# Kernel optimization log

Hardware: AMD Instinct MI355X
Metric: run time of the kernel (lower is better)

Reference implementation:

```python
import jax, jax.numpy as jnp
import numpy as np

DIM = 1024
NUM_HEADS = 16
HEAD_DIM = DIM // NUM_HEADS
EPS = 1e-6


def _rmsnorm(x, w):
    # x: [B,H,N,D], w: [D]
    var = jnp.mean(x * x, axis=-1, keepdims=True)
    return x * jax.lax.rsqrt(var + EPS) * w


def _rotary(x, cos, sin):
    # x: [B,H,N,D]; cos/sin: [1,1,N,D/2]; complex-pair rotation (llama style)
    x2 = x.reshape(*x.shape[:-1], HEAD_DIM // 2, 2)
    xr, xi = x2[..., 0], x2[..., 1]
    or_ = xr * cos - xi * sin
    oi_ = xr * sin + xi * cos
    return jnp.stack([or_, oi_], axis=-1).reshape(x.shape)


def setup_inputs() -> dict:
    key = jax.random.key(0)
    ks = jax.random.split(key, 6)
    B, N = 2, 2048
    x = jax.random.normal(ks[0], (B, N, DIM), dtype=jnp.float32)
    pos = jax.random.uniform(ks[1], (N, HEAD_DIM // 2), dtype=jnp.float32)  # rotary angles
    s_in = 1.0 / np.sqrt(DIM)
    qkv_w = jax.random.normal(ks[2], (3 * DIM, DIM), dtype=jnp.float32) * s_in
    q_norm_w = jnp.ones((HEAD_DIM,), dtype=jnp.float32)
    k_norm_w = jnp.ones((HEAD_DIM,), dtype=jnp.float32)
    proj_w = jax.random.normal(ks[3], (DIM, DIM), dtype=jnp.float32) * s_in
    proj_b = jnp.zeros((DIM,), dtype=jnp.float32)
    return {"x": x, "pos": pos, "qkv_w": qkv_w, "q_norm_w": q_norm_w,
            "k_norm_w": k_norm_w, "proj_w": proj_w, "proj_b": proj_b}


def reference(x, pos, qkv_w, q_norm_w, k_norm_w, proj_w, proj_b):
    B, N, C = x.shape
    H, D = NUM_HEADS, HEAD_DIM
    scale = D ** -0.5
    # QKV projection: [B,N,3C] -> [3,B,H,N,D]
    qkv = jnp.einsum('bnc,fc->bnf', x, qkv_w)
    qkv = qkv.reshape(B, N, 3, H, D).transpose(2, 0, 3, 1, 4)
    q, k, v = qkv[0], qkv[1], qkv[2]
    # QK RMSNorm over head_dim
    q = _rmsnorm(q, q_norm_w)
    k = _rmsnorm(k, k_norm_w)
    # Rotary embedding (freqs_cis = exp(i * pos))
    cos = jnp.cos(pos)[None, None, :, :]
    sin = jnp.sin(pos)[None, None, :, :]
    q = _rotary(q, cos, sin)
    k = _rotary(k, cos, sin)
    # Scaled dot-product attention (non-causal)
    scores = jnp.einsum('bhnd,bhmd->bhnm', q, k) * scale
    attn = jax.nn.softmax(scores, axis=-1)
    out = jnp.einsum('bhnm,bhmd->bhnd', attn, v)
    out = out.transpose(0, 2, 1, 3).reshape(B, N, C)
    return jnp.einsum('bnc,oc->bno', out, proj_w) + proj_b
```

## Files before the change

### kernel.cpp

```cpp
#include <hip/hip_runtime.h>
#include <hip/hip_bf16.h>

typedef unsigned short ushort_t;
using floatx4 = __attribute__((__ext_vector_type__(4))) float;
using bf16x8  = __attribute__((__ext_vector_type__(8))) __bf16;
using ushort4v = __attribute__((__ext_vector_type__(4))) ushort_t;

__device__ __forceinline__ unsigned int pkbf(float a, float b) {
  __hip_bfloat162 h = __float22bfloat162_rn(make_float2(a, b));
  unsigned int u;
  __builtin_memcpy(&u, &h, 4);
  return u;
}

__device__ __forceinline__ void gl2lds16(const ushort_t* g, ushort_t* l) {
  __builtin_amdgcn_global_load_lds(
      (const __attribute__((address_space(1))) unsigned int*)g,
      (__attribute__((address_space(3))) unsigned int*)l, 16, 0, 0);
}

__global__ void cast_all(const float* __restrict__ x, const float* __restrict__ qw,
                         const float* __restrict__ pw, ushort_t* __restrict__ ob,
                         const float* __restrict__ pos, float* __restrict__ cs) {
  const int T1 = 4096 * 1024, T2 = T1 + 3072 * 1024, T3 = T2 + 1024 * 1024;
  const int tid = blockIdx.x * blockDim.x + threadIdx.x;
  if (tid < 65536) {
    const float a = pos[tid];
    cs[2 * tid]     = __cosf(a);
    cs[2 * tid + 1] = __sinf(a);
  }
  const int i = tid * 4;
  if (i < T3) {
    const float* src = (i < T1) ? (x + i) : (i < T2) ? (qw + (i - T1)) : (pw + (i - T2));
    float4 v = *reinterpret_cast<const float4*>(src);
    uint2 o = make_uint2(pkbf(v.x, v.y), pkbf(v.z, v.w));
    *reinterpret_cast<uint2*>(&ob[i]) = o;
  }
}

__global__ __launch_bounds__(256)
void gemm_qkv_fused(const ushort_t* __restrict__ A, const ushort_t* __restrict__ B,
                    const float* __restrict__ cs,
                    const float* __restrict__ qnw, const float* __restrict__ knw,
                    ushort_t* __restrict__ qr, ushort_t* __restrict__ kr,
                    ushort_t* __restrict__ vt) {
  const int K = 1024;
  __shared__ __align__(16) ushort_t smem[16384];
  ushort_t* sA = smem;
  ushort_t* sB = smem + 8192;
  const int m0 = blockIdx.x * 128, n0 = blockIdx.y * 128;
  const int tid = threadIdx.x;
  const int lane = tid & 63, w = tid >> 6;
  const int wm = (w >> 1) * 64;
  const int grp = lane >> 4, l16 = lane & 15;
  const int r8 = lane >> 3;
  const int c8 = ((lane & 7) ^ r8) * 8;
  floatx4 acc[4][4] = {};
  for (int k0 = 0; k0 < K; k0 += 64) {
    __syncthreads();
#pragma unroll
    for (int i = 0; i < 4; i++) {
      const int j = w * 4 + i;
      gl2lds16(&A[(size_t)(m0 + j * 8 + r8) * K + k0 + c8], &sA[j * 512]);
      gl2lds16(&B[(size_t)(n0 + j * 8 + r8) * K + k0 + c8], &sB[j * 512]);
    }
    __syncthreads();
#pragma unroll
    for (int kk = 0; kk < 2; kk++) {
      bf16x8 af[4], bfr[4];
#pragma unroll
      for (int i = 0; i < 4; i++) {
        const int ra = wm + i * 16 + l16;
        af[i] = *reinterpret_cast<const bf16x8*>(
            &sA[ra * 64 + (((kk * 4 + grp) ^ (ra & 7)) << 3)]);
      }
#pragma unroll
      for (int i = 0; i < 4; i++) {
        const int rb = (w & 1) * 64 + i * 16 + l16;
        bfr[i] = *reinterpret_cast<const bf16x8*>(
            &sB[rb * 64 + (((kk * 4 + grp) ^ (rb & 7)) << 3)]);
      }
#pragma unroll
      for (int i = 0; i < 4; i++)
#pragma unroll
        for (int j = 0; j < 4; j++)
          acc[i][j] = __builtin_amdgcn_mfma_f32_16x16x32_bf16(af[i], bfr[j], acc[i][j], 0, 0, 0);
    }
  }
  __syncthreads();
  ushort_t* sE = smem + w * 4096;
  const int region = n0 >> 10;
  const int h = ((n0 & 1023) >> 6) + (w & 1);
  const int tbase = m0 + wm;
  const int bb = tbase >> 11;
  const int nwin = tbase & 2047;
  const int q = lane & 7;
  const int lr = lane >> 3;

  if (region < 2) {
    float* sEf = (float*)sE;
    const float* nwp = (region == 0) ? qnw : knw;
    const float qmul = (region == 0) ? 0.125f * 1.44269504088896340736f : 1.0f;
    float wgt[8];
    *(float4*)&wgt[0] = *(const float4*)&nwp[q * 8];
    *(float4*)&wgt[4] = *(const float4*)&nwp[q * 8 + 4];
#pragma unroll
    for (int hf = 0; hf < 2; hf++) {
      __builtin_amdgcn_s_waitcnt(0);
#pragma unroll
      for (int i2 = 0; i2 < 2; i2++)
#pragma unroll
        for (int rr = 0; rr < 4; rr++) {
          const int t2 = i2 * 16 + grp * 4 + rr;
#pragma unroll
          for (int j = 0; j < 4; j++) {
            const int cd = (j * 4 + (l16 >> 2)) ^ (t2 & 15);
            sEf[t2 * 64 + cd * 4 + (l16 & 3)] = acc[hf * 2 + i2][j][rr];
          }
        }
      __builtin_amdgcn_s_waitcnt(0);
#pragma unroll
      for (int tg = 0; tg < 4; tg++) {
        const int t2 = tg * 8 + lr;
        const int n = (tbase + hf * 32 + t2) & 2047;
        float v0[8];
        const int ck1 = (2 * q) ^ (t2 & 15), ck2 = (2 * q + 1) ^ (t2 & 15);
        *(float4*)&v0[0] = *(const float4*)&sEf[t2 * 64 + ck1 * 4];
        *(float4*)&v0[4] = *(const float4*)&sEf[t2 * 64 + ck2 * 4];
        float ss = 0.f;
#pragma unroll
        for (int e = 0; e < 8; e++) ss += v0[e] * v0[e];
        ss += __shfl_xor(ss, 1); ss += __shfl_xor(ss, 2); ss += __shfl_xor(ss, 4);
        const float rn = rsqrtf(ss * (1.0f / 64.0f) + 1e-6f);
        float4 c01 = *(const float4*)&cs[(n * 32 + q * 4) * 2];
        float4 c23 = *(const float4*)&cs[(n * 32 + q * 4) * 2 + 4];
        float ccv[4] = {c01.x, c01.z, c23.x, c23.z};
        float snv[4] = {c01.y, c01.w, c23.y, c23.w};
        union { unsigned int u32[4]; uint4 v4; } ov;
#pragma unroll
        for (int p = 0; p < 4; p++) {
          const float cc = ccv[p], sn = snv[p];
          const float xr = v0[2 * p] * rn * wgt[2 * p];
          const float xi = v0[2 * p + 1] * rn * wgt[2 * p + 1];
          ov.u32[p] = pkbf((xr * cc - xi * sn) * qmul, (xr * sn + xi * cc) * qmul);
        }
        const size_t rowb = ((size_t)(bb * 16 + h) * 2048 + n) * 64;
        if (region == 0)
          *reinterpret_cast<uint4*>(&qr[rowb + q * 8]) = ov.v4;
        else
          *reinterpret_cast<uint4*>(&kr[rowb + (q ^ (n & 7)) * 8]) = ov.v4;
      }
    }
  } else {
#pragma unroll
    for (int i = 0; i < 4; i++)
#pragma unroll
      for (int j = 0; j < 4; j++) {
        const int d = j * 16 + l16;
        const int ct = (i * 4 + grp) ^ (d & 15);
        uint2 pk = make_uint2(pkbf(acc[i][j][0], acc[i][j][1]),
                              pkbf(acc[i][j][2], acc[i][j][3]));
        *reinterpret_cast<uint2*>(&sE[d * 64 + ct * 4]) = pk;
      }
    __builtin_amdgcn_s_waitcnt(0);
#pragma unroll
    for (int dd = 0; dd < 8; dd++) {
      const int d = dd * 8 + lr;
      const int cta = 8 * (q >> 2) + (q & 3);
      union { ushort4v hh[2]; uint4 v4; } ob;
      ob.hh[0] = *reinterpret_cast<const ushort4v*>(&sE[d * 64 + ((cta ^ (d & 15)) * 4)]);
      ob.hh[1] = *reinterpret_cast<const ushort4v*>(&sE[d * 64 + (((cta + 4) ^ (d & 15)) * 4)]);
      *reinterpret_cast<uint4*>(
          &vt[((size_t)(bb * 16 + h) * 64 + d) * 2048 + nwin + (q ^ (d & 7)) * 8]) = ob.v4;
    }
  }
}

__global__ __launch_bounds__(512)
void flash_attn(const ushort_t* __restrict__ qr, const ushort_t* __restrict__ kr,
                const ushort_t* __restrict__ vt, ushort_t* __restrict__ aout) {
  const int bh = blockIdx.x;
  const int w = threadIdx.x >> 6, lane = threadIdx.x & 63;
  const int grp = lane >> 4, l16 = lane & 15;
  const int sw = l16 & 7;
  const int q0 = blockIdx.y * 128 + w * 16;
  const size_t hb = (size_t)bh * 2048 * 64;

  __shared__ ushort_t sK[2][128 * 64];
  __shared__ ushort_t sV[2][64 * 128];

  const ushort_t* qp = &qr[hb + (size_t)(q0 + l16) * 64 + grp * 8];
  const bf16x8 qa0 = *reinterpret_cast<const bf16x8*>(qp);
  const bf16x8 qa1 = *reinterpret_cast<const bf16x8*>(qp + 32);

  floatx4 o[4] = {};
  floatx4 ol = {};

  union { ushort_t u[8]; bf16x8 v; } onef;
#pragma unroll
  for (int e = 0; e < 8; e++) onef.u[e] = 0x3F80;

  auto stage = [&](int buf, int k0) {
    const ushort_t* kg = &kr[hb + (size_t)k0 * 64];
#pragma unroll
    for (int i = 0; i < 2; i++) {
      const int j = w * 2 + i;
      gl2lds16(kg + j * 512 + lane * 8, &sK[buf][j * 512]);
    }
#pragma unroll
    for (int i = 0; i < 2; i++) {
      const int d = (w * 2 + i) * 4;
      gl2lds16(&vt[((size_t)bh * 64 + d + (lane >> 4)) * 2048 + k0 + (lane & 15) * 8],
               &sV[buf][d * 128]);
    }
  };

  stage(0, 0);
  const int g0 = (grp ^ sw) * 8;
  for (int it = 0; it < 16; it++) {
    const int cur = it & 1;
    __syncthreads();
    if (it + 1 < 16) stage(1 - cur, (it + 1) * 128);
#pragma unroll
    for (int hh = 0; hh < 2; hh++) {
      const ushort_t* kb = &sK[cur][hh * 64 * 64];
      const ushort_t* vb = &sV[cur][hh * 64];
      floatx4 s[4];
#pragma unroll
      for (int nt = 0; nt < 4; nt++) {
        const ushort_t* kp = kb + (nt * 16 + l16) * 64;
        bf16x8 kf0 = *reinterpret_cast<const bf16x8*>(kp + g0);
        bf16x8 kf1 = *reinterpret_cast<const bf16x8*>(kp + (g0 ^ 32));
        floatx4 acc = {};
        acc = __builtin_amdgcn_mfma_f32_16x16x32_bf16(kf0, qa0, acc, 0, 0, 0);
        acc = __builtin_amdgcn_mfma_f32_16x16x32_bf16(kf1, qa1, acc, 0, 0, 0);
        s[nt] = acc;
      }
      float p[4][4];
#pragma unroll
      for (int nt = 0; nt < 4; nt++)
#pragma unroll
        for (int r = 0; r < 4; r++)
          p[nt][r] = __builtin_amdgcn_exp2f(s[nt][r]);
      union { unsigned int u32[4]; bf16x8 v; } pf[2];
#pragma unroll
      for (int c = 0; c < 2; c++) {
        pf[c].u32[0] = pkbf(p[2 * c][0], p[2 * c][1]);
        pf[c].u32[1] = pkbf(p[2 * c][2], p[2 * c][3]);
        pf[c].u32[2] = pkbf(p[2 * c + 1][0], p[2 * c + 1][1]);
        pf[c].u32[3] = pkbf(p[2 * c + 1][2], p[2 * c + 1][3]);
      }
#pragma unroll
      for (int c = 0; c < 2; c++) {
        ol = __builtin_amdgcn_mfma_f32_16x16x32_bf16(onef.v, pf[c].v, ol, 0, 0, 0);
#pragma unroll
        for (int dt = 0; dt < 4; dt++) {
          const bf16x8 vv = *reinterpret_cast<const bf16x8*>(
              vb + (dt * 16 + l16) * 128 + (((c * 4 + grp) ^ sw) << 3));
          o[dt] = __builtin_amdgcn_mfma_f32_16x16x32_bf16(vv, pf[c].v, o[dt], 0, 0, 0);
        }
      }
    }
  }
  const int b = bh >> 4, h = bh & 15;
  const float rl = 1.0f / ol[0];
  const size_t orow = (size_t)(b * 2048 + q0 + l16) * 1024 + h * 64;
#pragma unroll
  for (int dt = 0; dt < 4; dt++) {
    uint2 ov = make_uint2(pkbf(o[dt][0] * rl, o[dt][1] * rl),
                          pkbf(o[dt][2] * rl, o[dt][3] * rl));
    *reinterpret_cast<uint2*>(&aout[orow + dt * 16 + grp * 4]) = ov;
  }
}

__global__ __launch_bounds__(256)
void gemm_proj(const ushort_t* __restrict__ A, const ushort_t* __restrict__ B,
               float* __restrict__ Cout, const float* __restrict__ bias) {
  const int K = 1024, N = 1024;
  __shared__ __align__(16) ushort_t sA[8192];
  __shared__ __align__(16) ushort_t sB[4096];
  __shared__ float sT[4][2048];
  const int m0 = blockIdx.x * 128, n0 = blockIdx.y * 64;
  const int tid = threadIdx.x;
  const int lane = tid & 63, w = tid >> 6;
  const int wm = (w >> 1) * 64, wn = (w & 1) * 32;
  const int grp = lane >> 4, l16 = lane & 15;
  const int r8 = lane >> 3;
  const int c8 = ((lane & 7) ^ r8) * 8;
  floatx4 acc[4][2] = {};
  for (int k0 = 0; k0 < K; k0 += 64) {
    __syncthreads();
#pragma unroll
    for (int i = 0; i < 4; i++) {
      const int j = w * 4 + i;
      gl2lds16(&A[(size_t)(m0 + j * 8 + r8) * K + k0 + c8], &sA[j * 512]);
    }
#pragma unroll
    for (int i = 0; i < 2; i++) {
      const int j = w * 2 + i;
      gl2lds16(&B[(size_t)(n0 + j * 8 + r8) * K + k0 + c8], &sB[j * 512]);
    }
    __syncthreads();
#pragma unroll
    for (int kk = 0; kk < 2; kk++) {
      bf16x8 af[4], bfr[2];
#pragma unroll
      for (int i = 0; i < 4; i++) {
        const int ra = wm + i * 16 + l16;
        af[i] = *reinterpret_cast<const bf16x8*>(
            &sA[ra * 64 + (((kk * 4 + grp) ^ (ra & 7)) << 3)]);
      }
#pragma unroll
      for (int j = 0; j < 2; j++) {
        const int rb = wn + j * 16 + l16;
        bfr[j] = *reinterpret_cast<const bf16x8*>(
            &sB[rb * 64 + (((kk * 4 + grp) ^ (rb & 7)) << 3)]);
      }
#pragma unroll
      for (int i = 0; i < 4; i++)
#pragma unroll
        for (int j = 0; j < 2; j++)
          acc[i][j] = __builtin_amdgcn_mfma_f32_16x16x32_bf16(af[i], bfr[j], acc[i][j], 0, 0, 0);
    }
  }
  float bv[2];
#pragma unroll
  for (int j = 0; j < 2; j++) bv[j] = bias[n0 + wn + j * 16 + l16];
#pragma unroll
  for (int i = 0; i < 4; i++)
#pragma unroll
    for (int j = 0; j < 2; j++) {
      const int col = j * 16 + l16, c4 = col >> 2;
#pragma unroll
      for (int rr = 0; rr < 4; rr++) {
        const int row = i * 16 + grp * 4 + rr;
        sT[w][row * 32 + ((c4 ^ (row & 7)) << 2) + (col & 3)] = acc[i][j][rr] + bv[j];
      }
    }
  __builtin_amdgcn_s_waitcnt(0);
  const int lr = lane >> 3, ch = lane & 7;
#pragma unroll
  for (int rg = 0; rg < 8; rg++) {
    const int row = rg * 8 + lr;
    float4 vvv = *(const float4*)&sT[w][row * 32 + ((ch ^ (row & 7)) << 2)];
    *reinterpret_cast<float4*>(&Cout[(size_t)(m0 + wm + row) * N + n0 + wn + ch * 4]) = vvv;
  }
}

extern "C" void kernel_launch(void* const* d_in, const int* in_sizes, int n_in,
                              void* d_out, int out_size, void* d_ws, size_t ws_size,
                              hipStream_t stream) {
  const float* x      = (const float*)d_in[0];
  const float* pos    = (const float*)d_in[1];
  const float* qkv_w  = (const float*)d_in[2];
  const float* q_nw   = (const float*)d_in[3];
  const float* k_nw   = (const float*)d_in[4];
  const float* proj_w = (const float*)d_in[5];
  const float* proj_b = (const float*)d_in[6];
  float* out = (float*)d_out;

  ushort_t* x_b     = (ushort_t*)d_ws;
  ushort_t* qkvw_b  = x_b     + (size_t)4096 * 1024;
  ushort_t* projw_b = qkvw_b  + (size_t)3072 * 1024;
  ushort_t* q_r     = projw_b + (size_t)1024 * 1024;
  ushort_t* k_r     = q_r     + (size_t)32 * 2048 * 64;
  ushort_t* v_t     = k_r     + (size_t)32 * 2048 * 64;
  ushort_t* a_out   = v_t     + (size_t)32 * 2048 * 64;
  float*    cs_tab  = (float*)(a_out + (size_t)4096 * 1024);

  cast_all<<<8388608 / 4 / 256, 256, 0, stream>>>(x, qkv_w, proj_w, x_b, pos, cs_tab);

  gemm_qkv_fused<<<dim3(4096 / 128, 3072 / 128), 256, 0, stream>>>(
      x_b, qkvw_b, cs_tab, q_nw, k_nw, q_r, k_r, v_t);

  flash_attn<<<dim3(32, 2048 / 128), 512, 0, stream>>>(q_r, k_r, v_t, a_out);

  gemm_proj<<<dim3(4096 / 128, 1024 / 64), 256, 0, stream>>>(a_out, projw_b, out, proj_b);
}
```

Baseline: 188.9 us.

## Use 8 waves per block in QKV and projection GEMMs with smaller per-wave tiles

Both GEMM kernels move from 4 to 8 waves per block. Each wave now computes half as many rows (32 instead of 64), so per-wave accumulator registers drop and the tile loads are split across more threads. The QKV epilogue (norm/rotary and V transpose) is reworked for the 32-row wave tile. The projection GEMM now reuses the operand shared memory for its output staging, which cuts its LDS footprint. The aim is more latency hiding per CU, at the cost of less register-level reuse of B fragments per wave and more LDS reads per MFMA.

```diff
diff --git a/kernel.cpp b/kernel.cpp
--- a/kernel.cpp
+++ b/kernel.cpp
@@ -38,7 +38,7 @@
   }
 }
 
-__global__ __launch_bounds__(256)
+__global__ __launch_bounds__(512)
 void gemm_qkv_fused(const ushort_t* __restrict__ A, const ushort_t* __restrict__ B,
                     const float* __restrict__ cs,
                     const float* __restrict__ qnw, const float* __restrict__ knw,
@@ -51,49 +51,48 @@
   const int m0 = blockIdx.x * 128, n0 = blockIdx.y * 128;
   const int tid = threadIdx.x;
   const int lane = tid & 63, w = tid >> 6;
-  const int wm = (w >> 1) * 64;
+  const int wm = (w >> 1) * 32;
   const int grp = lane >> 4, l16 = lane & 15;
   const int r8 = lane >> 3;
   const int c8 = ((lane & 7) ^ r8) * 8;
-  floatx4 acc[4][4] = {};
+  floatx4 acc[2][4] = {};
   for (int k0 = 0; k0 < K; k0 += 64) {
     __syncthreads();
 #pragma unroll
-    for (int i = 0; i < 4; i++) {
-      const int j = w * 4 + i;
+    for (int i = 0; i < 2; i++) {
+      const int j = w * 2 + i;
       gl2lds16(&A[(size_t)(m0 + j * 8 + r8) * K + k0 + c8], &sA[j * 512]);
       gl2lds16(&B[(size_t)(n0 + j * 8 + r8) * K + k0 + c8], &sB[j * 512]);
     }
     __syncthreads();
 #pragma unroll
     for (int kk = 0; kk < 2; kk++) {
-      bf16x8 af[4], bfr[4];
-#pragma unroll
-      for (int i = 0; i < 4; i++) {
+      bf16x8 af[2], bfr[4];
+#pragma unroll
+      for (int i = 0; i < 2; i++) {
         const int ra = wm + i * 16 + l16;
         af[i] = *reinterpret_cast<const bf16x8*>(
             &sA[ra * 64 + (((kk * 4 + grp) ^ (ra & 7)) << 3)]);
       }
 #pragma unroll
-      for (int i = 0; i < 4; i++) {
-        const int rb = (w & 1) * 64 + i * 16 + l16;
-        bfr[i] = *reinterpret_cast<const bf16x8*>(
+      for (int j = 0; j < 4; j++) {
+        const int rb = (w & 1) * 64 + j * 16 + l16;
+        bfr[j] = *reinterpret_cast<const bf16x8*>(
             &sB[rb * 64 + (((kk * 4 + grp) ^ (rb & 7)) << 3)]);
       }
 #pragma unroll
-      for (int i = 0; i < 4; i++)
+      for (int i = 0; i < 2; i++)
 #pragma unroll
         for (int j = 0; j < 4; j++)
           acc[i][j] = __builtin_amdgcn_mfma_f32_16x16x32_bf16(af[i], bfr[j], acc[i][j], 0, 0, 0);
     }
   }
   __syncthreads();
-  ushort_t* sE = smem + w * 4096;
+  ushort_t* sE = smem + w * 2048;
   const int region = n0 >> 10;
   const int h = ((n0 & 1023) >> 6) + (w & 1);
   const int tbase = m0 + wm;
   const int bb = tbase >> 11;
-  const int nwin = tbase & 2047;
   const int q = lane & 7;
   const int lr = lane >> 3;
 
@@ -105,26 +104,24 @@
     *(float4*)&wgt[0] = *(const float4*)&nwp[q * 8];
     *(float4*)&wgt[4] = *(const float4*)&nwp[q * 8 + 4];
 #pragma unroll
-    for (int hf = 0; hf < 2; hf++) {
+    for (int p = 0; p < 2; p++) {
       __builtin_amdgcn_s_waitcnt(0);
 #pragma unroll
-      for (int i2 = 0; i2 < 2; i2++)
-#pragma unroll
-        for (int rr = 0; rr < 4; rr++) {
-          const int t2 = i2 * 16 + grp * 4 + rr;
-#pragma unroll
-          for (int j = 0; j < 4; j++) {
-            const int cd = (j * 4 + (l16 >> 2)) ^ (t2 & 15);
-            sEf[t2 * 64 + cd * 4 + (l16 & 3)] = acc[hf * 2 + i2][j][rr];
-          }
+      for (int rr = 0; rr < 4; rr++) {
+        const int t2 = grp * 4 + rr;
+#pragma unroll
+        for (int j = 0; j < 4; j++) {
+          const int cd = (j * 4 + (l16 >> 2)) ^ t2;
+          sEf[t2 * 64 + cd * 4 + (l16 & 3)] = acc[p][j][rr];
         }
+      }
       __builtin_amdgcn_s_waitcnt(0);
 #pragma unroll
-      for (int tg = 0; tg < 4; tg++) {
+      for (int tg = 0; tg < 2; tg++) {
         const int t2 = tg * 8 + lr;
-        const int n = (tbase + hf * 32 + t2) & 2047;
+        const int n = (tbase + p * 16 + t2) & 2047;
         float v0[8];
-        const int ck1 = (2 * q) ^ (t2 & 15), ck2 = (2 * q + 1) ^ (t2 & 15);
+        const int ck1 = (2 * q) ^ t2, ck2 = (2 * q + 1) ^ t2;
         *(float4*)&v0[0] = *(const float4*)&sEf[t2 * 64 + ck1 * 4];
         *(float4*)&v0[4] = *(const float4*)&sEf[t2 * 64 + ck2 * 4];
         float ss = 0.f;
@@ -138,11 +135,11 @@
         float snv[4] = {c01.y, c01.w, c23.y, c23.w};
         union { unsigned int u32[4]; uint4 v4; } ov;
 #pragma unroll
-        for (int p = 0; p < 4; p++) {
-          const float cc = ccv[p], sn = snv[p];
-          const float xr = v0[2 * p] * rn * wgt[2 * p];
-          const float xi = v0[2 * p + 1] * rn * wgt[2 * p + 1];
-          ov.u32[p] = pkbf((xr * cc - xi * sn) * qmul, (xr * sn + xi * cc) * qmul);
+        for (int pp = 0; pp < 4; pp++) {
+          const float cc = ccv[pp], sn = snv[pp];
+          const float xr = v0[2 * pp] * rn * wgt[2 * pp];
+          const float xi = v0[2 * pp + 1] * rn * wgt[2 * pp + 1];
+          ov.u32[pp] = pkbf((xr * cc - xi * sn) * qmul, (xr * sn + xi * cc) * qmul);
         }
         const size_t rowb = ((size_t)(bb * 16 + h) * 2048 + n) * 64;
         if (region == 0)
@@ -152,26 +149,29 @@
       }
     }
   } else {
-#pragma unroll
-    for (int i = 0; i < 4; i++)
+    const int nw_ = tbase & 2047;
+    const int n64 = nw_ & ~63;
+    const int hw = (nw_ >> 5) & 1;
+#pragma unroll
+    for (int i = 0; i < 2; i++)
 #pragma unroll
       for (int j = 0; j < 4; j++) {
         const int d = j * 16 + l16;
-        const int ct = (i * 4 + grp) ^ (d & 15);
+        const int ct = (grp * 2 + i) ^ (d & 7);
         uint2 pk = make_uint2(pkbf(acc[i][j][0], acc[i][j][1]),
                               pkbf(acc[i][j][2], acc[i][j][3]));
-        *reinterpret_cast<uint2*>(&sE[d * 64 + ct * 4]) = pk;
+        *reinterpret_cast<uint2*>(&sE[d * 32 + ct * 4]) = pk;
       }
     __builtin_amdgcn_s_waitcnt(0);
-#pragma unroll
-    for (int dd = 0; dd < 8; dd++) {
-      const int d = dd * 8 + lr;
-      const int cta = 8 * (q >> 2) + (q & 3);
+    const int lc = lane & 3;
+#pragma unroll
+    for (int dd = 0; dd < 4; dd++) {
+      const int d = dd * 16 + (lane >> 2);
       union { ushort4v hh[2]; uint4 v4; } ob;
-      ob.hh[0] = *reinterpret_cast<const ushort4v*>(&sE[d * 64 + ((cta ^ (d & 15)) * 4)]);
-      ob.hh[1] = *reinterpret_cast<const ushort4v*>(&sE[d * 64 + (((cta + 4) ^ (d & 15)) * 4)]);
+      ob.hh[0] = *reinterpret_cast<const ushort4v*>(&sE[d * 32 + (((2 * lc) ^ (d & 7)) * 4)]);
+      ob.hh[1] = *reinterpret_cast<const ushort4v*>(&sE[d * 32 + (((2 * lc + 1) ^ (d & 7)) * 4)]);
       *reinterpret_cast<uint4*>(
-          &vt[((size_t)(bb * 16 + h) * 64 + d) * 2048 + nwin + (q ^ (d & 7)) * 8]) = ob.v4;
+          &vt[((size_t)(bb * 16 + h) * 64 + d) * 2048 + n64 + (((hw * 4 + lc) ^ (d & 7)) * 8)]) = ob.v4;
     }
   }
 }
@@ -273,39 +273,35 @@
   }
 }
 
-__global__ __launch_bounds__(256)
+__global__ __launch_bounds__(512)
 void gemm_proj(const ushort_t* __restrict__ A, const ushort_t* __restrict__ B,
                float* __restrict__ Cout, const float* __restrict__ bias) {
   const int K = 1024, N = 1024;
-  __shared__ __align__(16) ushort_t sA[8192];
-  __shared__ __align__(16) ushort_t sB[4096];
-  __shared__ float sT[4][2048];
+  __shared__ __align__(16) ushort_t smem[16384];
+  ushort_t* sA = smem;
+  ushort_t* sB = smem + 8192;
   const int m0 = blockIdx.x * 128, n0 = blockIdx.y * 64;
   const int tid = threadIdx.x;
   const int lane = tid & 63, w = tid >> 6;
-  const int wm = (w >> 1) * 64, wn = (w & 1) * 32;
+  const int wm = (w >> 1) * 32, wn = (w & 1) * 32;
   const int grp = lane >> 4, l16 = lane & 15;
   const int r8 = lane >> 3;
   const int c8 = ((lane & 7) ^ r8) * 8;
-  floatx4 acc[4][2] = {};
+  floatx4 acc[2][2] = {};
   for (int k0 = 0; k0 < K; k0 += 64) {
     __syncthreads();
-#pragma unroll
-    for (int i = 0; i < 4; i++) {
-      const int j = w * 4 + i;
-      gl2lds16(&A[(size_t)(m0 + j * 8 + r8) * K + k0 + c8], &sA[j * 512]);
-    }
 #pragma unroll
     for (int i = 0; i < 2; i++) {
       const int j = w * 2 + i;
-      gl2lds16(&B[(size_t)(n0 + j * 8 + r8) * K + k0 + c8], &sB[j * 512]);
-    }
+      gl2lds16(&A[(size_t)(m0 + j * 8 + r8) * K + k0 + c8], &sA[j * 512]);
+    }
+    gl2lds16(&B[(size_t)(n0 + w * 8 + r8) * K + k0 + c8], &sB[w * 512]);
     __syncthreads();
 #pragma unroll
     for (int kk = 0; kk < 2; kk++) {
-      bf16x8 af[4], bfr[2];
-#pragma unroll
-      for (int i = 0; i < 4; i++) {
+      bf16x8 af[2], bfr[2];
+#pragma unroll
+      for (int i = 0; i < 2; i++) {
         const int ra = wm + i * 16 + l16;
         af[i] = *reinterpret_cast<const bf16x8*>(
             &sA[ra * 64 + (((kk * 4 + grp) ^ (ra & 7)) << 3)]);
@@ -317,32 +313,34 @@
             &sB[rb * 64 + (((kk * 4 + grp) ^ (rb & 7)) << 3)]);
       }
 #pragma unroll
-      for (int i = 0; i < 4; i++)
+      for (int i = 0; i < 2; i++)
 #pragma unroll
         for (int j = 0; j < 2; j++)
           acc[i][j] = __builtin_amdgcn_mfma_f32_16x16x32_bf16(af[i], bfr[j], acc[i][j], 0, 0, 0);
     }
   }
+  __syncthreads();
+  float* sT = (float*)(smem + w * 2048);
   float bv[2];
 #pragma unroll
   for (int j = 0; j < 2; j++) bv[j] = bias[n0 + wn + j * 16 + l16];
 #pragma unroll
-  for (int i = 0; i < 4; i++)
+  for (int i = 0; i < 2; i++)
 #pragma unroll
     for (int j = 0; j < 2; j++) {
       const int col = j * 16 + l16, c4 = col >> 2;
 #pragma unroll
       for (int rr = 0; rr < 4; rr++) {
         const int row = i * 16 + grp * 4 + rr;
-        sT[w][row * 32 + ((c4 ^ (row & 7)) << 2) + (col & 3)] = acc[i][j][rr] + bv[j];
+        sT[row * 32 + ((c4 ^ (row & 7)) << 2) + (col & 3)] = acc[i][j][rr] + bv[j];
       }
     }
   __builtin_amdgcn_s_waitcnt(0);
   const int lr = lane >> 3, ch = lane & 7;
 #pragma unroll
-  for (int rg = 0; rg < 8; rg++) {
+  for (int rg = 0; rg < 4; rg++) {
     const int row = rg * 8 + lr;
-    float4 vvv = *(const float4*)&sT[w][row * 32 + ((ch ^ (row & 7)) << 2)];
+    float4 vvv = *(const float4*)&sT[row * 32 + ((ch ^ (row & 7)) << 2)];
     *reinterpret_cast<float4*>(&Cout[(size_t)(m0 + wm + row) * N + n0 + wn + ch * 4]) = vvv;
   }
 }
@@ -370,10 +368,10 @@
 
   cast_all<<<8388608 / 4 / 256, 256, 0, stream>>>(x, qkv_w, proj_w, x_b, pos, cs_tab);
 
-  gemm_qkv_fused<<<dim3(4096 / 128, 3072 / 128), 256, 0, stream>>>(
+  gemm_qkv_fused<<<dim3(4096 / 128, 3072 / 128), 512, 0, stream>>>(
       x_b, qkvw_b, cs_tab, q_nw, k_nw, q_r, k_r, v_t);
 
   flash_attn<<<dim3(32, 2048 / 128), 512, 0, stream>>>(q_r, k_r, v_t, a_out);
 
-  gemm_proj<<<dim3(4096 / 128, 1024 / 64), 256, 0, stream>>>(a_out, projw_b, out, proj_b);
-}
+  gemm_proj<<<dim3(4096 / 128, 1024 / 64), 512, 0, stream>>>(a_out, projw_b, out, proj_b);
+}
```

Result: faster. 180.0 us, median of 2 (-4.7%).
